# Performance work log

Measured on AMD Instinct MI355X. Metric: run time of the kernel, lower is better.

The kernel has to match this reference:

```python
import jax, jax.numpy as jnp
import numpy as np

EPS = 1e-08
ORDINAL = 2.0

def setup_inputs() -> dict:
    key = jax.random.key(0)
    k1, k2, k3, k4, k5 = jax.random.split(key, 5)
    B, IN, OUT = 1024, 256, 1024
    inputs = jax.random.normal(k1, (B, IN), dtype=jnp.float32)
    weights = jax.random.normal(k2, (OUT, IN), dtype=jnp.float32) * (1.0 / np.sqrt(IN))
    biases = jax.random.normal(k3, (OUT,), dtype=jnp.float32) * (1.0 / np.sqrt(IN))
    centers = jax.random.normal(k4, (OUT, IN), dtype=jnp.float32) * 0.1
    # diag inv covars ~ U(3/(IN+0.5), 3/(IN-0.5)) per reset_parameters
    inv_covars = jax.random.uniform(k5, (OUT, IN), dtype=jnp.float32,
                                    minval=3.0 / (IN + 0.5), maxval=3.0 / (IN - 0.5))
    return {"inputs": inputs, "weights": weights, "biases": biases,
            "centers": centers, "inv_covars": inv_covars}

def reference(inputs, weights, biases, centers, inv_covars):
    # linear part: [B, OUT]
    l = inputs @ weights.T + biases
    # diag covar path (ordinal = 2.0, so the 1e-32 stabilizer is absent and
    # pow(c^2, 1/ordinal) == |c| after clamping):
    # g[b, z] = sum_i ( |x[b,i] - c[z,i]| * sqrt(clamp(ic[z,i])^2) )^2
    ic = jnp.minimum(inv_covars, 1.0 / EPS)
    scale = jnp.power(ic * ic, 1.0 / ORDINAL)  # [OUT, IN]
    diff = jnp.abs(inputs[:, None, :] - centers[None, :, :]) * scale[None, :, :]  # [B, OUT, IN]
    g = jnp.exp(-jnp.sum(jnp.power(diff, ORDINAL), axis=-1))  # [B, OUT]
    res = l * g
    return (res, g)
```

## Files before the change

kernel.cpp:

```cpp
#include <hip/hip_runtime.h>
#include <math.h>


typedef __attribute__((ext_vector_type(8))) short short8;
typedef __attribute__((ext_vector_type(4))) float floatx4;

#define BDIM   1024
#define INDIM  256
#define OUTDIM 1024

__device__ __forceinline__ unsigned short f2bf(float f) {
    union { float f; unsigned u; } v; v.f = f;
    unsigned r = v.u + 0x7FFFu + ((v.u >> 16) & 1u);
    return (unsigned short)(r >> 16);
}

__device__ __forceinline__ void load8(const float* __restrict__ p, float f[8]) {
    float4 v0 = *(const float4*)p;
    float4 v1 = *(const float4*)(p + 4);
    f[0]=v0.x; f[1]=v0.y; f[2]=v0.z; f[3]=v0.w;
    f[4]=v1.x; f[5]=v1.y; f[6]=v1.z; f[7]=v1.w;
}

__device__ __forceinline__ short8 pack8(const float f[8]) {
    short8 r;
    #pragma unroll
    for (int i = 0; i < 8; ++i) r[i] = (short)f2bf(f[i]);
    return r;
}

#define MFMA __builtin_amdgcn_mfma_f32_16x16x32_bf16

__global__ __launch_bounds__(256)
void fgn_fused(const float* __restrict__ X, const float* __restrict__ W,
               const float* __restrict__ Bias, const float* __restrict__ C,
               const float* __restrict__ IC, float* __restrict__ Out)
{
    const int n0   = blockIdx.x * 32;
    const int m0   = blockIdx.y * 32;
    const int t    = threadIdx.x;
    const int w    = t >> 6;
    const int lane = t & 63;
    const int r    = lane & 15;
    const int q    = lane >> 4;

    __shared__ float sL[4 * 64 * 17];
    __shared__ float sG[4 * 64 * 17];
    __shared__ float sC[4][32];

    floatx4 zero = {0.f, 0.f, 0.f, 0.f};
    floatx4 accL[2][2] = {{zero, zero}, {zero, zero}};
    floatx4 accG[2][2] = {{zero, zero}, {zero, zero}};
    floatx4 accC[2]    = {zero, zero};

    short8 ones;
    #pragma unroll
    for (int i = 0; i < 8; ++i) ones[i] = (short)0x3F80;

    #pragma unroll
    for (int kk = 0; kk < 2; ++kk) {
        const int k = w * 64 + kk * 32 + q * 8;
        short8 a0[2], a2[2];
        #pragma unroll
        for (int mt = 0; mt < 2; ++mt) {
            float x[8], xs[8];
            load8(&X[(size_t)(m0 + mt * 16 + r) * INDIM + k], x);
            #pragma unroll
            for (int i = 0; i < 8; ++i) xs[i] = x[i] * x[i];
            a0[mt] = pack8(x);
            a2[mt] = pack8(xs);
        }
        #pragma unroll
        for (int nt = 0; nt < 2; ++nt) {
            const size_t ro = (size_t)(n0 + nt * 16 + r) * INDIM + k;
            float wv[8], cv[8], iv[8], g1[8], g2[8], g3[8];
            load8(&W[ro],  wv);
            load8(&C[ro],  cv);
            load8(&IC[ro], iv);
            #pragma unroll
            for (int i = 0; i < 8; ++i) {
                float s  = fminf(iv[i], 1e8f);
                float qq = s * s;
                g2[i] = qq;
                g1[i] = -2.f * cv[i] * qq;
                g3[i] = cv[i] * cv[i] * qq;
            }
            short8 wf = pack8(wv), f1 = pack8(g1), f2 = pack8(g2), f3 = pack8(g3);
            accL[0][nt] = MFMA(a0[0], wf, accL[0][nt], 0, 0, 0);
            accL[1][nt] = MFMA(a0[1], wf, accL[1][nt], 0, 0, 0);
            accG[0][nt] = MFMA(a0[0], f1, accG[0][nt], 0, 0, 0);
            accG[1][nt] = MFMA(a0[1], f1, accG[1][nt], 0, 0, 0);
            accG[0][nt] = MFMA(a2[0], f2, accG[0][nt], 0, 0, 0);
            accG[1][nt] = MFMA(a2[1], f2, accG[1][nt], 0, 0, 0);
            accC[nt]    = MFMA(ones,  f3, accC[nt],    0, 0, 0);
        }
    }

    #pragma unroll
    for (int mt = 0; mt < 2; ++mt)
        #pragma unroll
        for (int nt = 0; nt < 2; ++nt)
            #pragma unroll
            for (int reg = 0; reg < 4; ++reg) {
                const int f = mt * 8 + nt * 4 + reg;
                sG[(w * 64 + lane) * 17 + f] = accG[mt][nt][reg];
                sL[(w * 64 + lane) * 17 + f] = accL[mt][nt][reg];
            }
    if (q == 0) {
        sC[w][r]      = accC[0][0];
        sC[w][16 + r] = accC[1][0];
    }
    __syncthreads();

    const int l  = lane;
    const int li = l & 15;
    float cz0 = 0.f, cz1 = 0.f;
    #pragma unroll
    for (int ww = 0; ww < 4; ++ww) { cz0 += sC[ww][li]; cz1 += sC[ww][16 + li]; }
    const float bias0 = Bias[n0 + li], bias1 = Bias[n0 + 16 + li];
    float* OutR = Out;
    float* OutG = Out + (size_t)BDIM * OUTDIM;
    #pragma unroll
    for (int j = 0; j < 4; ++j) {
        const int f = w * 4 + j;
        float Ls = 0.f, Gs = 0.f;
        #pragma unroll
        for (int ww = 0; ww < 4; ++ww) {
            Ls += sL[(ww * 64 + l) * 17 + f];
            Gs += sG[(ww * 64 + l) * 17 + f];
        }
        const int mt = f >> 3, nt = (f >> 2) & 1, reg = f & 3;
        const int m = m0 + mt * 16 + (l >> 4) * 4 + reg;
        const int n = n0 + nt * 16 + li;
        const float g   = expf(-(Gs + (nt ? cz1 : cz0)));
        const float res = (Ls + (nt ? bias1 : bias0)) * g;
        OutR[(size_t)m * OUTDIM + n] = res;
        OutG[(size_t)m * OUTDIM + n] = g;
    }
}

extern "C" void kernel_launch(void* const* d_in, const int* in_sizes, int n_in,
                              void* d_out, int out_size, void* d_ws, size_t ws_size,
                              hipStream_t stream) {
    const float* X    = (const float*)d_in[0];
    const float* W    = (const float*)d_in[1];
    const float* Bias = (const float*)d_in[2];
    const float* C    = (const float*)d_in[3];
    const float* IC   = (const float*)d_in[4];
    float* Out = (float*)d_out;

    dim3 grid(OUTDIM / 32, BDIM / 32);
    fgn_fused<<<grid, 256, 0, stream>>>(X, W, Bias, C, IC, Out);
}
```

Measured before the change: 79.22 us.

## Stage bf16 tiles in LDS with a K loop instead of split-K across waves

Replaces the per-wave split-K scheme, where each wave read operands straight from global memory and partials were reduced through shared memory, with a K-loop over 64-wide tiles. Each iteration converts X, X², W and the center/covariance factors to bf16 once into padded LDS, and the waves read their MFMA operands from there. The output tile grows to 64x32, and each wave owns 16 rows, so the cross-wave reduction and its epilogue sync disappear. The cost is four K iterations with two barriers each and no overlap between global loads and the MFMAs, plus fewer blocks in the grid.

After: 71.58 us. 9.6% less time.

```diff
diff --git a/kernel.cpp b/kernel.cpp
--- a/kernel.cpp
+++ b/kernel.cpp
@@ -1,141 +1,149 @@
 #include <hip/hip_runtime.h>
+#include <hip/hip_bf16.h>
 #include <math.h>
 
 
 typedef __attribute__((ext_vector_type(8))) short short8;
 typedef __attribute__((ext_vector_type(4))) float floatx4;
 
-#define BDIM   1024
-#define INDIM  256
-#define OUTDIM 1024
+#define MFMA __builtin_amdgcn_mfma_f32_16x16x32_bf16
+#define INDIM 256
+#define OUTD  1024
+#define BD    1024
+#define TM 64
+#define TN 32
+#define TK 64
+#define KSTR 72
 
-__device__ __forceinline__ unsigned short f2bf(float f) {
-    union { float f; unsigned u; } v; v.f = f;
-    unsigned r = v.u + 0x7FFFu + ((v.u >> 16) & 1u);
-    return (unsigned short)(r >> 16);
+__device__ __forceinline__ unsigned pkbf(float a, float b) {
+    union { __hip_bfloat162 h; unsigned u; } v;
+    v.h = __float22bfloat162_rn(make_float2(a, b));
+    return v.u;
 }
-
-__device__ __forceinline__ void load8(const float* __restrict__ p, float f[8]) {
-    float4 v0 = *(const float4*)p;
-    float4 v1 = *(const float4*)(p + 4);
-    f[0]=v0.x; f[1]=v0.y; f[2]=v0.z; f[3]=v0.w;
-    f[4]=v1.x; f[5]=v1.y; f[6]=v1.z; f[7]=v1.w;
-}
-
-__device__ __forceinline__ short8 pack8(const float f[8]) {
-    short8 r;
-    #pragma unroll
-    for (int i = 0; i < 8; ++i) r[i] = (short)f2bf(f[i]);
-    return r;
-}
-
-#define MFMA __builtin_amdgcn_mfma_f32_16x16x32_bf16
 
 __global__ __launch_bounds__(256)
 void fgn_fused(const float* __restrict__ X, const float* __restrict__ W,
                const float* __restrict__ Bias, const float* __restrict__ C,
                const float* __restrict__ IC, float* __restrict__ Out)
 {
-    const int n0   = blockIdx.x * 32;
-    const int m0   = blockIdx.y * 32;
+    __shared__ __align__(16) unsigned short As [TM * KSTR];
+    __shared__ __align__(16) unsigned short As2[TM * KSTR];
+    __shared__ __align__(16) unsigned short Bw [TN * KSTR];
+    __shared__ __align__(16) unsigned short Bg1[TN * KSTR];
+    __shared__ __align__(16) unsigned short Bg2[TN * KSTR];
+    __shared__ __align__(16) unsigned short Bg3[TN * KSTR];
+
+    const int n0   = blockIdx.x * TN;
+    const int m0   = blockIdx.y * TM;
     const int t    = threadIdx.x;
     const int w    = t >> 6;
     const int lane = t & 63;
     const int r    = lane & 15;
     const int q    = lane >> 4;
 
-    __shared__ float sL[4 * 64 * 17];
-    __shared__ float sG[4 * 64 * 17];
-    __shared__ float sC[4][32];
+    const int arow = t >> 2;
+    const int akq  = (t & 3) << 4;
+    const int bz   = t >> 3;
+    const int bkq  = (t & 7) << 3;
 
     floatx4 zero = {0.f, 0.f, 0.f, 0.f};
-    floatx4 accL[2][2] = {{zero, zero}, {zero, zero}};
-    floatx4 accG[2][2] = {{zero, zero}, {zero, zero}};
-    floatx4 accC[2]    = {zero, zero};
-
+    floatx4 accL[2] = {zero, zero};
+    floatx4 accG[2] = {zero, zero};
+    floatx4 accC[2] = {zero, zero};
     short8 ones;
     #pragma unroll
     for (int i = 0; i < 8; ++i) ones[i] = (short)0x3F80;
 
-    #pragma unroll
-    for (int kk = 0; kk < 2; ++kk) {
-        const int k = w * 64 + kk * 32 + q * 8;
-        short8 a0[2], a2[2];
-        #pragma unroll
-        for (int mt = 0; mt < 2; ++mt) {
-            float x[8], xs[8];
-            load8(&X[(size_t)(m0 + mt * 16 + r) * INDIM + k], x);
+    for (int k0 = 0; k0 < INDIM; k0 += TK) {
+        float4 xa[4];
+        {
+            const float* xp = &X[(size_t)(m0 + arow) * INDIM + k0 + akq];
             #pragma unroll
-            for (int i = 0; i < 8; ++i) xs[i] = x[i] * x[i];
-            a0[mt] = pack8(x);
-            a2[mt] = pack8(xs);
+            for (int i = 0; i < 4; ++i) xa[i] = ((const float4*)xp)[i];
         }
-        #pragma unroll
-        for (int nt = 0; nt < 2; ++nt) {
-            const size_t ro = (size_t)(n0 + nt * 16 + r) * INDIM + k;
-            float wv[8], cv[8], iv[8], g1[8], g2[8], g3[8];
-            load8(&W[ro],  wv);
-            load8(&C[ro],  cv);
-            load8(&IC[ro], iv);
+        const size_t bo = (size_t)(n0 + bz) * INDIM + k0 + bkq;
+        float4 wv0 = *(const float4*)&W[bo],  wv1 = *(const float4*)&W[bo + 4];
+        float4 cv0 = *(const float4*)&C[bo],  cv1 = *(const float4*)&C[bo + 4];
+        float4 iv0 = *(const float4*)&IC[bo], iv1 = *(const float4*)&IC[bo + 4];
+
+        __syncthreads();
+
+        {
+            const float* xf = (const float*)xa;
+            unsigned ux[8], ux2[8];
             #pragma unroll
             for (int i = 0; i < 8; ++i) {
-                float s  = fminf(iv[i], 1e8f);
+                float e0 = xf[2*i], e1 = xf[2*i+1];
+                ux[i]  = pkbf(e0, e1);
+                ux2[i] = pkbf(e0 * e0, e1 * e1);
+            }
+            uint4* pa  = (uint4*)&As [arow * KSTR + akq];
+            uint4* pa2 = (uint4*)&As2[arow * KSTR + akq];
+            pa[0]  = make_uint4(ux[0],  ux[1],  ux[2],  ux[3]);
+            pa[1]  = make_uint4(ux[4],  ux[5],  ux[6],  ux[7]);
+            pa2[0] = make_uint4(ux2[0], ux2[1], ux2[2], ux2[3]);
+            pa2[1] = make_uint4(ux2[4], ux2[5], ux2[6], ux2[7]);
+        }
+        {
+            float wf[8] = {wv0.x,wv0.y,wv0.z,wv0.w, wv1.x,wv1.y,wv1.z,wv1.w};
+            float cf[8] = {cv0.x,cv0.y,cv0.z,cv0.w, cv1.x,cv1.y,cv1.z,cv1.w};
+            float f0[8] = {iv0.x,iv0.y,iv0.z,iv0.w, iv1.x,iv1.y,iv1.z,iv1.w};
+            float g1[8], g2[8], g3[8];
+            #pragma unroll
+            for (int i = 0; i < 8; ++i) {
+                float s  = fminf(f0[i], 1e8f);
                 float qq = s * s;
                 g2[i] = qq;
-                g1[i] = -2.f * cv[i] * qq;
-                g3[i] = cv[i] * cv[i] * qq;
+                g1[i] = -2.f * cf[i] * qq;
+                g3[i] = cf[i] * cf[i] * qq;
             }
-            short8 wf = pack8(wv), f1 = pack8(g1), f2 = pack8(g2), f3 = pack8(g3);
-            accL[0][nt] = MFMA(a0[0], wf, accL[0][nt], 0, 0, 0);
-            accL[1][nt] = MFMA(a0[1], wf, accL[1][nt], 0, 0, 0);
-            accG[0][nt] = MFMA(a0[0], f1, accG[0][nt], 0, 0, 0);
-            accG[1][nt] = MFMA(a0[1], f1, accG[1][nt], 0, 0, 0);
-            accG[0][nt] = MFMA(a2[0], f2, accG[0][nt], 0, 0, 0);
-            accG[1][nt] = MFMA(a2[1], f2, accG[1][nt], 0, 0, 0);
-            accC[nt]    = MFMA(ones,  f3, accC[nt],    0, 0, 0);
+            const int bb = bz * KSTR + bkq;
+            *(uint4*)&Bw [bb] = make_uint4(pkbf(wf[0],wf[1]), pkbf(wf[2],wf[3]),
+                                           pkbf(wf[4],wf[5]), pkbf(wf[6],wf[7]));
+            *(uint4*)&Bg1[bb] = make_uint4(pkbf(g1[0],g1[1]), pkbf(g1[2],g1[3]),
+                                           pkbf(g1[4],g1[5]), pkbf(g1[6],g1[7]));
+            *(uint4*)&Bg2[bb] = make_uint4(pkbf(g2[0],g2[1]), pkbf(g2[2],g2[3]),
+                                           pkbf(g2[4],g2[5]), pkbf(g2[6],g2[7]));
+            *(uint4*)&Bg3[bb] = make_uint4(pkbf(g3[0],g3[1]), pkbf(g3[2],g3[3]),
+                                           pkbf(g3[4],g3[5]), pkbf(g3[6],g3[7]));
+        }
+        __syncthreads();
+
+        #pragma unroll
+        for (int kk = 0; kk < 2; ++kk) {
+            const int ko = kk * 32 + q * 8;
+            short8 a0 = *(const short8*)&As [(w * 16 + r) * KSTR + ko];
+            short8 a2 = *(const short8*)&As2[(w * 16 + r) * KSTR + ko];
+            #pragma unroll
+            for (int nt = 0; nt < 2; ++nt) {
+                const int br = (nt * 16 + r) * KSTR + ko;
+                short8 bwf = *(const short8*)&Bw [br];
+                short8 b1f = *(const short8*)&Bg1[br];
+                short8 b2f = *(const short8*)&Bg2[br];
+                short8 b3f = *(const short8*)&Bg3[br];
+                accL[nt] = MFMA(a0,   bwf, accL[nt], 0, 0, 0);
+                accG[nt] = MFMA(a0,   b1f, accG[nt], 0, 0, 0);
+                accG[nt] = MFMA(a2,   b2f, accG[nt], 0, 0, 0);
+                accC[nt] = MFMA(ones, b3f, accC[nt], 0, 0, 0);
+            }
         }
     }
 
+    float* OutR = Out;
+    float* OutG = Out + (size_t)BD * OUTD;
     #pragma unroll
-    for (int mt = 0; mt < 2; ++mt)
+    for (int nt = 0; nt < 2; ++nt) {
+        const int n     = n0 + nt * 16 + r;
+        const float bias = Bias[n];
+        const float cz   = accC[nt][0];
         #pragma unroll
-        for (int nt = 0; nt < 2; ++nt)
-            #pragma unroll
-            for (int reg = 0; reg < 4; ++reg) {
-                const int f = mt * 8 + nt * 4 + reg;
-                sG[(w * 64 + lane) * 17 + f] = accG[mt][nt][reg];
-                sL[(w * 64 + lane) * 17 + f] = accL[mt][nt][reg];
-            }
-    if (q == 0) {
-        sC[w][r]      = accC[0][0];
-        sC[w][16 + r] = accC[1][0];
-    }
-    __syncthreads();
-
-    const int l  = lane;
-    const int li = l & 15;
-    float cz0 = 0.f, cz1 = 0.f;
-    #pragma unroll
-    for (int ww = 0; ww < 4; ++ww) { cz0 += sC[ww][li]; cz1 += sC[ww][16 + li]; }
-    const float bias0 = Bias[n0 + li], bias1 = Bias[n0 + 16 + li];
-    float* OutR = Out;
-    float* OutG = Out + (size_t)BDIM * OUTDIM;
-    #pragma unroll
-    for (int j = 0; j < 4; ++j) {
-        const int f = w * 4 + j;
-        float Ls = 0.f, Gs = 0.f;
-        #pragma unroll
-        for (int ww = 0; ww < 4; ++ww) {
-            Ls += sL[(ww * 64 + l) * 17 + f];
-            Gs += sG[(ww * 64 + l) * 17 + f];
+        for (int reg = 0; reg < 4; ++reg) {
+            const int m = m0 + w * 16 + q * 4 + reg;
+            const float g   = expf(-(accG[nt][reg] + cz));
+            const float res = (accL[nt][reg] + bias) * g;
+            OutR[(size_t)m * OUTD + n] = res;
+            OutG[(size_t)m * OUTD + n] = g;
         }
-        const int mt = f >> 3, nt = (f >> 2) & 1, reg = f & 3;
-        const int m = m0 + mt * 16 + (l >> 4) * 4 + reg;
-        const int n = n0 + nt * 16 + li;
-        const float g   = expf(-(Gs + (nt ? cz1 : cz0)));
-        const float res = (Ls + (nt ? bias1 : bias0)) * g;
-        OutR[(size_t)m * OUTDIM + n] = res;
-        OutG[(size_t)m * OUTDIM + n] = g;
     }
 }
 
@@ -149,6 +157,6 @@
     const float* IC   = (const float*)d_in[4];
     float* Out = (float*)d_out;
 
-    dim3 grid(OUTDIM / 32, BDIM / 32);
+    dim3 grid(OUTD / TN, BD / TM);
     fgn_fused<<<grid, 256, 0, stream>>>(X, W, Bias, C, IC, Out);
 }
```
